# Performance work log

Hardware: AMD Instinct MI355X
Metric: run time of the kernel (lower is better)

The kernel has to match this reference:

```python
import jax, jax.numpy as jnp
import numpy as np

B, T, H, V = 32, 16, 768, 32000
EPS = 1e-5


def _conv(x, w, stride, pad):
    return jax.lax.conv_general_dilated(
        x, w, (stride, stride), [(pad, pad), (pad, pad)],
        dimension_numbers=('NCHW', 'OIHW', 'NCHW'))


def _bn(x, g, b, m, v):
    inv = g / jnp.sqrt(v + EPS)
    return x * inv[None, :, None, None] + (b - m * inv)[None, :, None, None]


def setup_inputs() -> dict:
    key = jax.random.key(0)
    ks = iter(jax.random.split(key, 48))

    def rn(shape, s=0.02):
        return s * jax.random.normal(next(ks), shape, jnp.float32)

    def bn_params(c):
        g = 1.0 + 0.1 * jax.random.normal(next(ks), (c,), jnp.float32)
        b = 0.1 * jax.random.normal(next(ks), (c,), jnp.float32)
        m = 0.1 * jax.random.normal(next(ks), (c,), jnp.float32)
        v = jax.random.uniform(next(ks), (c,), jnp.float32, 0.5, 1.5)
        return g, b, m, v

    inp = {}
    inp['images'] = jax.random.normal(next(ks), (B, 3, 224, 224), jnp.float32)
    inp['captions'] = jax.random.randint(next(ks), (B, T), 0, V)

    inp['conv1_w'] = rn((64, 3, 7, 7))
    inp['bn1_g'], inp['bn1_b'], inp['bn1_m'], inp['bn1_v'] = bn_params(64)
    inp['conv2_w'] = rn((128, 64, 3, 3))
    inp['bn2_g'], inp['bn2_b'], inp['bn2_m'], inp['bn2_v'] = bn_params(128)
    inp['conv3_w'] = rn((256, 128, 3, 3))
    inp['bn3_g'], inp['bn3_b'], inp['bn3_m'], inp['bn3_v'] = bn_params(256)
    inp['conv4_w'] = rn((H, 256, 3, 3))
    inp['bn4_g'], inp['bn4_b'], inp['bn4_m'], inp['bn4_v'] = bn_params(H)

    emb = rn((V, H), 1.0)
    inp['emb_table'] = emb.at[0].set(0.0)  # padding_idx=0 row is zero
    inp['attn_w'] = rn((H, H))             # attn_proj (no bias)
    inp['w_ih'] = rn((4 * H, 2 * H))       # LSTM input weights (i,f,g,o)
    inp['w_hh'] = rn((4 * H, H))
    inp['b_ih'] = rn((4 * H,))
    inp['b_hh'] = rn((4 * H,))
    inp['fc_w'] = rn((V, H))
    inp['fc_b'] = rn((V,))
    return inp


def _forward(images, captions, conv1_w, bn1_g, bn1_b, bn1_m, bn1_v,
             conv2_w, bn2_g, bn2_b, bn2_m, bn2_v,
             conv3_w, bn3_g, bn3_b, bn3_m, bn3_v,
             conv4_w, bn4_g, bn4_b, bn4_m, bn4_v,
             emb_table, attn_w, w_ih, w_hh, b_ih, b_hh, fc_w, fc_b):
    # ---- ResNetEncoder ----
    x = jax.nn.relu(_bn(_conv(images, conv1_w, 2, 3), bn1_g, bn1_b, bn1_m, bn1_v))
    x = jax.lax.reduce_window(x, -jnp.inf, jax.lax.max, (1, 1, 3, 3), (1, 1, 2, 2),
                              ((0, 0), (0, 0), (1, 1), (1, 1)))
    x = jax.nn.relu(_bn(_conv(x, conv2_w, 1, 1), bn2_g, bn2_b, bn2_m, bn2_v))
    x = jax.nn.relu(_bn(_conv(x, conv3_w, 2, 1), bn3_g, bn3_b, bn3_m, bn3_v))
    x = jax.nn.relu(_bn(_conv(x, conv4_w, 1, 1), bn4_g, bn4_b, bn4_m, bn4_v))
    b, c, hh, ww = x.shape
    memory = x.reshape(b, c, hh * ww).transpose(0, 2, 1)[:, :196, :]  # [B,196,H]

    # ---- LSTMAttnDecoder ----
    emb = emb_table[captions]  # [B,T,H]
    h0 = jnp.zeros((b, H), jnp.float32)
    c0 = jnp.zeros((b, H), jnp.float32)

    def step(carry, e_t):
        h, cst = carry
        q = h @ attn_w.T                                    # [B,H]
        scores = jnp.einsum('bh,bmh->bm', q, memory)        # [B,196]
        ctx = jnp.einsum('bm,bmh->bh', jax.nn.softmax(scores, axis=-1), memory)
        xin = jnp.concatenate([e_t, ctx], axis=-1)          # [B,2H]
        gates = xin @ w_ih.T + b_ih + h @ w_hh.T + b_hh     # [B,4H]
        i, f, g, o = jnp.split(gates, 4, axis=-1)
        c_new = jax.nn.sigmoid(f) * cst + jax.nn.sigmoid(i) * jnp.tanh(g)
        h_new = jax.nn.sigmoid(o) * jnp.tanh(c_new)
        logits = h_new @ fc_w.T + fc_b                      # [B,V]
        return (h_new, c_new), logits

    (hT, cT), logits = jax.lax.scan(step, (h0, c0), emb.transpose(1, 0, 2))
    logits = logits.transpose(1, 0, 2)  # [B,T,V]
    return logits, (hT[None], cT[None])


def reference(images, captions, conv1_w, bn1_g, bn1_b, bn1_m, bn1_v,
              conv2_w, bn2_g, bn2_b, bn2_m, bn2_v,
              conv3_w, bn3_g, bn3_b, bn3_m, bn3_v,
              conv4_w, bn4_g, bn4_b, bn4_m, bn4_v,
              emb_table, attn_w, w_ih, w_hh, b_ih, b_hh, fc_w, fc_b):
    return _forward(images, captions, conv1_w, bn1_g, bn1_b, bn1_m, bn1_v,
                    conv2_w, bn2_g, bn2_b, bn2_m, bn2_v,
                    conv3_w, bn3_g, bn3_b, bn3_m, bn3_v,
                    conv4_w, bn4_g, bn4_b, bn4_m, bn4_v,
                    emb_table, attn_w, w_ih, w_hh, b_ih, b_hh, fc_w, fc_b)
```

## Files before the change

### kernel.cpp

```cpp
#include <hip/hip_runtime.h>
#include <math.h>

#define NB 32
#define NT 16
#define NH 768
#define NV 32000

typedef short bf16x8 __attribute__((ext_vector_type(8)));
typedef float floatx4 __attribute__((ext_vector_type(4)));
typedef unsigned short ushort_t;

__device__ __forceinline__ float bf2f(unsigned short h) {
    unsigned u = ((unsigned)h) << 16;
    return __builtin_bit_cast(float, u);
}
__device__ __forceinline__ unsigned short f2bf(float f) {
    unsigned u = __builtin_bit_cast(unsigned, f);
    u += 0x7fffu + ((u >> 16) & 1u);
    return (unsigned short)(u >> 16);
}
__device__ __forceinline__ float sigmoidf_(float x) { return 1.f / (1.f + expf(-x)); }

__device__ __forceinline__ bf16x8 cvt8(float4 a, float4 b) {
    bf16x8 t;
    t[0] = (short)f2bf(a.x); t[1] = (short)f2bf(a.y);
    t[2] = (short)f2bf(a.z); t[3] = (short)f2bf(a.w);
    t[4] = (short)f2bf(b.x); t[5] = (short)f2bf(b.y);
    t[6] = (short)f2bf(b.z); t[7] = (short)f2bf(b.w);
    return t;
}

__global__ __launch_bounds__(256) void bn_prep4(
    const float* __restrict__ g1, const float* __restrict__ b1, const float* __restrict__ m1, const float* __restrict__ v1,
    const float* __restrict__ g2, const float* __restrict__ b2, const float* __restrict__ m2, const float* __restrict__ v2,
    const float* __restrict__ g3, const float* __restrict__ b3, const float* __restrict__ m3, const float* __restrict__ v3,
    const float* __restrict__ g4, const float* __restrict__ b4, const float* __restrict__ m4, const float* __restrict__ v4,
    float* __restrict__ s1, float* __restrict__ o1, float* __restrict__ s2, float* __restrict__ o2,
    float* __restrict__ s3, float* __restrict__ o3, float* __restrict__ s4, float* __restrict__ o4) {
    int i = blockIdx.x * 256 + threadIdx.x;
    const float *g, *b, *m, *v;
    float *s, *o;
    int c;
    if (i < 64)        { g = g1; b = b1; m = m1; v = v1; s = s1; o = o1; c = i; }
    else if (i < 192)  { g = g2; b = b2; m = m2; v = v2; s = s2; o = o2; c = i - 64; }
    else if (i < 448)  { g = g3; b = b3; m = m3; v = v3; s = s3; o = o3; c = i - 192; }
    else if (i < 1216) { g = g4; b = b4; m = m4; v = v4; s = s4; o = o4; c = i - 448; }
    else return;
    float inv = g[c] * rsqrtf(v[c] + 1e-5f);
    s[c] = inv;
    o[c] = b[c] - m[c] * inv;
}

__global__ __launch_bounds__(256) void zfill(unsigned long long* __restrict__ p, long long n) {
    long long i = (long long)blockIdx.x * 256 + threadIdx.x;
    if (i < n) p[i] = 0ULL;
}

__global__ __launch_bounds__(256) void cvt_b16rows(const float* __restrict__ src, ushort_t* __restrict__ dst,
                                                   int cols8, int ldsrc, int total8) {
    int i = blockIdx.x * 256 + threadIdx.x;
    if (i >= total8) return;
    int r = i / cols8, g = i % cols8;
    const float4* s = (const float4*)(src + (size_t)r * ldsrc + g * 8);
    float4 a = s[0], b = s[1];
    *(bf16x8*)(dst + (size_t)i * 8) = cvt8(a, b);
}

__global__ __launch_bounds__(256) void cvt_packW_conv(const float* __restrict__ w, ushort_t* __restrict__ dst,
                                                      int CIN, int total) {
    int idx = blockIdx.x * 256 + threadIdx.x;
    if (idx >= total) return;
    int e = idx & 7, lane = (idx >> 3) & 63, j = (idx >> 9) & 3;
    int r = idx >> 11;
    int KQ = CIN >> 5;
    int kq = r % KQ; r /= KQ;
    int tap = r % 9; int nt = r / 9;
    int co = nt * 64 + j * 16 + (lane & 15);
    int ci = kq * 32 + (lane >> 4) * 8 + e;
    dst[idx] = f2bf(w[((size_t)co * CIN + ci) * 9 + tap]);
}

__global__ __launch_bounds__(256) void cvt_wcombP(const float* __restrict__ w_ih, const float* __restrict__ w_hh,
                                                  ushort_t* __restrict__ dst) {
    int idx = blockIdx.x * 256 + threadIdx.x;
    if (idx >= 3072 * 1536) return;
    int e = idx & 7, lane = (idx >> 3) & 63;
    int t = idx >> 9;
    int kq = t % 48, gg = t / 48;
    int g = gg & 3, bx = gg >> 2;
    int j = g * 768 + bx * 16 + (lane & 15);
    int k = kq * 32 + (lane >> 4) * 8 + e;
    float v = (k < NH) ? w_ih[(size_t)j * (2 * NH) + NH + k] : w_hh[(size_t)j * NH + (k - NH)];
    dst[idx] = f2bf(v);
}

__global__ __launch_bounds__(256) void cvt_wattnTP(const float* __restrict__ w, ushort_t* __restrict__ dst) {
    int idx = blockIdx.x * 256 + threadIdx.x;
    if (idx >= 768 * 768) return;
    int e = idx & 7, lane = (idx >> 3) & 63, j = (idx >> 9) & 3;
    int t = idx >> 11;
    int kq = t % 24, nt = t / 24;
    int n = nt * 64 + 16 * j + (lane & 15);
    int k = kq * 32 + (lane >> 4) * 8 + e;
    dst[idx] = f2bf(w[(size_t)k * 768 + n]);
}

__global__ __launch_bounds__(256) void cvt_pad(const float* __restrict__ src, ushort_t* __restrict__ dst) {
    int idx = blockIdx.x * 256 + threadIdx.x;
    if (idx >= 64 * 160) return;
    int co = idx / 160, k = idx % 160;
    dst[idx] = (k < 147) ? f2bf(src[co * 147 + k]) : (ushort_t)0;
}

__global__ __launch_bounds__(256) void im2col1(const float* __restrict__ img, ushort_t* __restrict__ A) {
    int idx = blockIdx.x * 256 + threadIdx.x;
    const int total = 121856 * 160;
    if (idx >= total) return;
    int k = idx % 160;
    int m = idx / 160;
    ushort_t v = 0;
    if (k < 147) {
        int b = m / 3808;
        int rm = m % 3808;
        int y = rm / 112, x = rm % 112;
        int ci = k / 49;
        int r = k % 49;
        int ky = r / 7, kx = r % 7;
        int iy = 2 * y - 3 + ky;
        int ix = 2 * x - 3 + kx;
        if ((unsigned)iy < 224u && (unsigned)ix < 224u)
            v = f2bf(img[((size_t)(b * 3 + ci) * 224 + iy) * 224 + ix]);
    }
    A[idx] = v;
}

__global__ __launch_bounds__(256) void conv1_gemm(
    const ushort_t* __restrict__ A, const ushort_t* __restrict__ Bw,
    const float* __restrict__ scale, const float* __restrict__ bias,
    ushort_t* __restrict__ out) {
    int lane = threadIdx.x & 63, w = threadIdx.x >> 6;
    int m0 = (blockIdx.x * 4 + w) * 64;
    int lr = lane & 15, kl = (lane >> 4) * 8;
    floatx4 acc[4][4];
    #pragma unroll
    for (int i = 0; i < 4; ++i)
        #pragma unroll
        for (int j = 0; j < 4; ++j) acc[i][j] = 0.f;
    #pragma unroll
    for (int k0 = 0; k0 < 160; k0 += 32) {
        bf16x8 a[4], bb[4];
        #pragma unroll
        for (int i = 0; i < 4; ++i) a[i] = *(const bf16x8*)(A + (size_t)(m0 + 16 * i + lr) * 160 + kl + k0);
        #pragma unroll
        for (int j = 0; j < 4; ++j) bb[j] = *(const bf16x8*)(Bw + (size_t)(16 * j + lr) * 160 + kl + k0);
        #pragma unroll
        for (int i = 0; i < 4; ++i)
            #pragma unroll
            for (int j = 0; j < 4; ++j)
                acc[i][j] = __builtin_amdgcn_mfma_f32_16x16x32_bf16(a[i], bb[j], acc[i][j], 0, 0, 0);
    }
    #pragma unroll
    for (int i = 0; i < 4; ++i) {
        #pragma unroll
        for (int r = 0; r < 4; ++r) {
            int m = m0 + 16 * i + (lane >> 4) * 4 + r;
            int b = m / 3808;
            int rm = m % 3808;
            int y = rm / 112, x = rm % 112;
            #pragma unroll
            for (int j = 0; j < 4; ++j) {
                int n = 16 * j + lr;
                float v = fmaxf(acc[i][j][r] * scale[n] + bias[n], 0.f);
                out[((size_t)(b * 34 + y) * 112 + x) * 64 + n] = f2bf(v);
            }
        }
    }
}

__global__ __launch_bounds__(256) void pool_kernel(const ushort_t* __restrict__ in,
                                                   ushort_t* __restrict__ hal2) {
    int idx = blockIdx.x * 256 + threadIdx.x;
    const int total = 32 * 17 * 56 * 8;
    if (idx >= total) return;
    int c8 = idx & 7;
    int rest = idx >> 3;
    int x = rest % 56; rest /= 56;
    int y = rest % 17; int b = rest / 17;
    float mx[8];
    #pragma unroll
    for (int j = 0; j < 8; ++j) mx[j] = -INFINITY;
    for (int dy = -1; dy <= 1; ++dy) {
        int iy = 2 * y + dy;
        if ((unsigned)iy >= 34u) continue;
        for (int dx = -1; dx <= 1; ++dx) {
            int ix = 2 * x + dx;
            if ((unsigned)ix >= 112u) continue;
            bf16x8 v = *(const bf16x8*)(in + (((size_t)(b * 34 + iy)) * 112 + ix) * 64 + c8 * 8);
            #pragma unroll
            for (int j = 0; j < 8; ++j) mx[j] = fmaxf(mx[j], bf2f((unsigned short)v[j]));
        }
    }
    bf16x8 o;
    #pragma unroll
    for (int j = 0; j < 8; ++j) o[j] = (short)f2bf(mx[j]);
    *(bf16x8*)(hal2 + (((size_t)(b * 19 + y + 1)) * 58 + (x + 1)) * 64 + c8 * 8) = o;
}

template <int CIN, int HH, int WH, int STRIDE, int HOUT, int WOUT, int COUT, int MEMOUT, int OH, int OW>
__global__ __launch_bounds__(64) void conv_mfma(
    const ushort_t* __restrict__ in, const ushort_t* __restrict__ wtP,
    const float* __restrict__ scale, const float* __restrict__ bias,
    ushort_t* __restrict__ out) {
    int lane = threadIdx.x;
    int mt = blockIdx.x, nt = blockIdx.y;
    int lr = lane & 15, kl = (lane >> 4) * 8;
    int rowoff[4];
    #pragma unroll
    for (int i = 0; i < 4; ++i) {
        int m = mt * 64 + 16 * i + lr;
        int b = m / (HOUT * WOUT);
        int rm = m % (HOUT * WOUT);
        int y = rm / WOUT, x = rm % WOUT;
        rowoff[i] = ((b * HH + y * STRIDE) * WH + x * STRIDE) * CIN + kl;
    }
    floatx4 acc[4][4];
    #pragma unroll
    for (int i = 0; i < 4; ++i)
        #pragma unroll
        for (int j = 0; j < 4; ++j) acc[i][j] = 0.f;

    #pragma unroll
    for (int ky = 0; ky < 3; ++ky) {
        #pragma unroll
        for (int kx = 0; kx < 3; ++kx) {
            int ioff = (ky * WH + kx) * CIN;
            int t = ky * 3 + kx;
            #pragma unroll
            for (int k0 = 0; k0 < CIN; k0 += 32) {
                bf16x8 a[4], bb[4];
                #pragma unroll
                for (int i = 0; i < 4; ++i)
                    a[i] = *(const bf16x8*)(in + rowoff[i] + ioff + k0);
                #pragma unroll
                for (int j = 0; j < 4; ++j)
                    bb[j] = *(const bf16x8*)(wtP + ((((size_t)(nt * 9 + t) * (CIN / 32) + (k0 >> 5)) * 4 + j) * 64 + lane) * 8);
                #pragma unroll
                for (int i = 0; i < 4; ++i)
                    #pragma unroll
                    for (int j = 0; j < 4; ++j)
                        acc[i][j] = __builtin_amdgcn_mfma_f32_16x16x32_bf16(a[i], bb[j], acc[i][j], 0, 0, 0);
            }
        }
    }
    #pragma unroll
    for (int i = 0; i < 4; ++i) {
        #pragma unroll
        for (int r = 0; r < 4; ++r) {
            int m = mt * 64 + 16 * i + (lane >> 4) * 4 + r;
            int b = m / (HOUT * WOUT);
            int rm = m % (HOUT * WOUT);
            int y = rm / WOUT, x = rm % WOUT;
            #pragma unroll
            for (int j = 0; j < 4; ++j) {
                int n = nt * 64 + 16 * j + lr;
                float v = fmaxf(acc[i][j][r] * scale[n] + bias[n], 0.f);
                ushort_t hv = f2bf(v);
                if (MEMOUT) {
                    out[(size_t)m * COUT + n] = hv;
                } else {
                    out[((size_t)(b * OH + y + 1) * OW + (x + 1)) * COUT + n] = hv;
                }
            }
        }
    }
}

__global__ __launch_bounds__(64) void kmat_gemm(
    const ushort_t* __restrict__ memv, const ushort_t* __restrict__ Bp,
    ushort_t* __restrict__ KT) {
    int lane = threadIdx.x;
    int mt = blockIdx.x, nt = blockIdx.y;
    int lr = lane & 15, kl = (lane >> 4) * 8;
    floatx4 acc[4][4];
    #pragma unroll
    for (int i = 0; i < 4; ++i)
        #pragma unroll
        for (int j = 0; j < 4; ++j) acc[i][j] = 0.f;
    for (int kq = 0; kq < 24; ++kq) {
        bf16x8 a[4], bb[4];
        #pragma unroll
        for (int i = 0; i < 4; ++i)
            a[i] = *(const bf16x8*)(memv + (size_t)(mt * 64 + 16 * i + lr) * 768 + kq * 32 + kl);
        #pragma unroll
        for (int j = 0; j < 4; ++j)
            bb[j] = *(const bf16x8*)(Bp + (((size_t)(nt * 24 + kq) * 4 + j) * 64 + lane) * 8);
        #pragma unroll
        for (int i = 0; i < 4; ++i)
            #pragma unroll
            for (int j = 0; j < 4; ++j)
                acc[i][j] = __builtin_amdgcn_mfma_f32_16x16x32_bf16(a[i], bb[j], acc[i][j], 0, 0, 0);
    }
    #pragma unroll
    for (int i = 0; i < 4; ++i) {
        #pragma unroll
        for (int r = 0; r < 4; ++r) {
            int mg = mt * 64 + 16 * i + (lane >> 4) * 4 + r;
            int b = mg / 196, m = mg % 196;
            #pragma unroll
            for (int j = 0; j < 4; ++j) {
                int n = nt * 64 + 16 * j + lr;
                KT[(((size_t)b * 96 + (n >> 3)) * 196 + m) * 8 + (n & 7)] = f2bf(acc[i][j][r]);
            }
        }
    }
}

__global__ __launch_bounds__(256) void gather_embP(const int* __restrict__ caps,
                                                   const float* __restrict__ table,
                                                   ushort_t* __restrict__ dst) {
    int idx = blockIdx.x * 256 + threadIdx.x;
    if (idx >= 512 * 768) return;
    int e = idx & 7, lane = (idx >> 3) & 63, i = (idx >> 9) & 3;
    int t2 = idx >> 11;
    int kq = t2 % 24, mt = t2 / 24;
    int r = mt * 64 + i * 16 + (lane & 15);
    int k = kq * 32 + (lane >> 4) * 8 + e;
    int t = r >> 5, b = r & 31;
    dst[idx] = f2bf(table[(size_t)caps[b * NT + t] * NH + k]);
}

template <int REMAP>
__global__ __launch_bounds__(256, 4) void gemm_ldsb(
    const ushort_t* __restrict__ Ap, const ushort_t* __restrict__ Bb,
    const float* __restrict__ bias1, const float* __restrict__ bias2,
    float* __restrict__ C, int N) {
    __shared__ ushort_t bt[2][64 * 72];
    int tid = threadIdx.x;
    int lane = tid & 63, w = tid >> 6;
    int nt = blockIdx.x, mh = blockIdx.y;
    int n0 = nt * 64;
    int mt = mh * 4 + w;
    int lr = lane & 15, hi = lane >> 4;
    int srow = tid >> 2, sc = tid & 3;
    const ushort_t* gsrc = Bb + (size_t)(n0 + srow) * 768 + sc * 8;
    int woff = srow * 72 + sc * 8;
    floatx4 acc[4][4];
    #pragma unroll
    for (int i = 0; i < 4; ++i)
        #pragma unroll
        for (int j = 0; j < 4; ++j) acc[i][j] = 0.f;
    bf16x8 s0 = *(const bf16x8*)(gsrc);
    bf16x8 s1 = *(const bf16x8*)(gsrc + 32);
    for (int kc = 0; kc < 12; ++kc) {
        ushort_t* bufw = &bt[kc & 1][0];
        *(bf16x8*)(bufw + woff) = s0;
        *(bf16x8*)(bufw + woff + 32) = s1;
        if (kc < 11) {
            const ushort_t* p = gsrc + (size_t)(kc + 1) * 64;
            s0 = *(const bf16x8*)(p);
            s1 = *(const bf16x8*)(p + 32);
        }
        __syncthreads();
        const ushort_t* bufr = &bt[kc & 1][0];
        #pragma unroll
        for (int kk = 0; kk < 2; ++kk) {
            int kq = kc * 2 + kk;
            bf16x8 bfr[4], a[4];
            #pragma unroll
            for (int j = 0; j < 4; ++j)
                bfr[j] = *(const bf16x8*)(bufr + (j * 16 + lr) * 72 + kk * 32 + hi * 8);
            #pragma unroll
            for (int i = 0; i < 4; ++i)
                a[i] = *(const bf16x8*)(Ap + ((((size_t)mt * 24 + kq) * 4 + i) * 64 + lane) * 8);
            #pragma unroll
            for (int i = 0; i < 4; ++i)
                #pragma unroll
                for (int j = 0; j < 4; ++j)
                    acc[i][j] = __builtin_amdgcn_mfma_f32_16x16x32_bf16(a[i], bfr[j], acc[i][j], 0, 0, 0);
        }
    }
    #pragma unroll
    for (int i = 0; i < 4; ++i) {
        #pragma unroll
        for (int rr = 0; rr < 4; ++rr) {
            int m = mt * 64 + 16 * i + hi * 4 + rr;
            #pragma unroll
            for (int j = 0; j < 4; ++j) {
                int n = n0 + 16 * j + lr;
                float vv = acc[i][j][rr];
                if (bias1) vv += bias1[n];
                if (bias2) vv += bias2[n];
                if (REMAP) {
                    int t = m >> 5, b = m & 31;
                    C[(size_t)((b << 4) + t) * NV + n] = vv;
                } else {
                    C[(size_t)m * N + n] = vv;
                }
            }
        }
    }
}

__global__ __launch_bounds__(768) void attn2(
    ushort_t* __restrict__ xin, const ushort_t* __restrict__ KT,
    const ushort_t* __restrict__ mem) {
    __shared__ float hq[NH];
    __shared__ float sl[196];
    __shared__ float red[16];
    int b = blockIdx.x, tid = threadIdx.x;
    hq[tid] = bf2f(xin[(size_t)b * 1536 + NH + tid]);
    __syncthreads();
    if (tid < 392) {
        int m = tid >> 1, half = tid & 1;
        const ushort_t* basep = KT + (((size_t)b * 96 + half * 48) * 196 + m) * 8;
        float acc = 0.f;
        #pragma unroll 4
        for (int k8 = 0; k8 < 48; ++k8) {
            bf16x8 v = *(const bf16x8*)(basep + (size_t)k8 * 196 * 8);
            const float* qp = hq + (half * 48 + k8) * 8;
            #pragma unroll
            for (int j = 0; j < 8; ++j)
                acc = fmaf(bf2f((unsigned short)v[j]), qp[j], acc);
        }
        acc += __shfl_xor(acc, 1);
        if (!half) sl[m] = acc;
    }
    __syncthreads();
    float sc = (tid < 196) ? sl[tid] : -INFINITY;
    float v = sc;
    #pragma unroll
    for (int off = 32; off; off >>= 1) v = fmaxf(v, __shfl_down(v, off));
    if ((tid & 63) == 0) red[tid >> 6] = v;
    __syncthreads();
    if (tid == 0) {
        float m = red[0];
        for (int i = 1; i < 12; ++i) m = fmaxf(m, red[i]);
        red[12] = m;
    }
    __syncthreads();
    float mx = red[12];
    float e = (tid < 196) ? expf(sc - mx) : 0.f;
    __syncthreads();
    v = e;
    #pragma unroll
    for (int off = 32; off; off >>= 1) v += __shfl_down(v, off);
    if ((tid & 63) == 0) red[tid >> 6] = v;
    __syncthreads();
    if (tid == 0) {
        float s = red[0];
        for (int i = 1; i < 12; ++i) s += red[i];
        red[12] = 1.f / s;
    }
    __syncthreads();
    if (tid < 196) sl[tid] = e * red[12];
    __syncthreads();
    {
        float acc = 0.f;
        const ushort_t* mb = mem + (size_t)b * 196 * NH + tid;
        #pragma unroll 4
        for (int m = 0; m < 196; ++m) acc = fmaf(sl[m], bf2f(mb[(size_t)m * NH]), acc);
        xin[(size_t)b * 1536 + tid] = f2bf(acc);
    }
}

__global__ __launch_bounds__(256) void step_fused(
    const ushort_t* __restrict__ xin_r, const ushort_t* __restrict__ wcombP,
    const float* __restrict__ eg_t,
    float* __restrict__ cbuf, float* __restrict__ hbuf,
    ushort_t* __restrict__ xin_w, ushort_t* __restrict__ hallP, int tstep) {
    __shared__ float pbuf[4][64][33];
    int lane = threadIdx.x & 63, w = threadIdx.x >> 6;
    int bx = blockIdx.x;
    int lr = lane & 15, kl = (lane >> 4) * 8;
    floatx4 acc[2][4];
    #pragma unroll
    for (int i = 0; i < 2; ++i)
        #pragma unroll
        for (int g = 0; g < 4; ++g) acc[i][g] = 0.f;
    for (int kq = 0; kq < 12; ++kq) {
        int k = w * 384 + kq * 32;
        bf16x8 a[2], bb[4];
        #pragma unroll
        for (int i = 0; i < 2; ++i)
            a[i] = *(const bf16x8*)(xin_r + (size_t)(16 * i + lr) * 1536 + k + kl);
        #pragma unroll
        for (int g = 0; g < 4; ++g)
            bb[g] = *(const bf16x8*)(wcombP + (((size_t)(bx * 4 + g) * 48 + (w * 12 + kq)) * 64 + lane) * 8);
        #pragma unroll
        for (int i = 0; i < 2; ++i)
            #pragma unroll
            for (int g = 0; g < 4; ++g)
                acc[i][g] = __builtin_amdgcn_mfma_f32_16x16x32_bf16(a[i], bb[g], acc[i][g], 0, 0, 0);
    }
    #pragma unroll
    for (int i = 0; i < 2; ++i)
        #pragma unroll
        for (int g = 0; g < 4; ++g)
            #pragma unroll
            for (int r = 0; r < 4; ++r) {
                int m = 16 * i + (lane >> 4) * 4 + r;
                pbuf[w][g * 16 + lr][m] = acc[i][g][r];
            }
    __syncthreads();
    int tid = threadIdx.x;
    #pragma unroll
    for (int o = 0; o < 2; ++o) {
        int pid = tid * 2 + o;
        int m = pid & 31, c = pid >> 5;
        int kcol = bx * 16 + c;
        float gi = 0.f, gf = 0.f, gg = 0.f, go = 0.f;
        #pragma unroll
        for (int ww = 0; ww < 4; ++ww) {
            gi += pbuf[ww][c][m];
            gf += pbuf[ww][16 + c][m];
            gg += pbuf[ww][32 + c][m];
            go += pbuf[ww][48 + c][m];
        }
        const float* eg = eg_t + (size_t)m * 3072;
        gi += eg[kcol];
        gf += eg[768 + kcol];
        gg += eg[1536 + kcol];
        go += eg[2304 + kcol];
        float cst = cbuf[m * 768 + kcol];
        float cn = sigmoidf_(gf) * cst + sigmoidf_(gi) * tanhf(gg);
        float hn = sigmoidf_(go) * tanhf(cn);
        cbuf[m * 768 + kcol] = cn;
        hbuf[m * 768 + kcol] = hn;
        ushort_t hb = f2bf(hn);
        xin_w[(size_t)m * 1536 + NH + kcol] = hb;
        int rrow = tstep * 32 + m;
        int mtp = rrow >> 6, ip = (rrow >> 4) & 3, lrp = rrow & 15;
        int kqp = kcol >> 5, hip = (kcol >> 3) & 3, ep = kcol & 7;
        hallP[((((size_t)mtp * 24 + kqp) * 4 + ip) * 64 + (lrp | (hip << 4))) * 8 + ep] = hb;
    }
}

__global__ __launch_bounds__(256) void zero_state(float* __restrict__ h, float* __restrict__ c,
                                                  ushort_t* __restrict__ xin) {
    int i = blockIdx.x * 256 + threadIdx.x;
    if (i < NB * 1536) xin[i] = 0;
    if (i < NB * NH) { h[i] = 0.f; c[i] = 0.f; }
}

__global__ __launch_bounds__(256) void copy_hc(const float* __restrict__ h, const float* __restrict__ c,
                                               float* __restrict__ out) {
    int i = blockIdx.x * 256 + threadIdx.x;
    if (i < NB * NH) {
        out[(size_t)NB * NT * NV + i] = h[i];
        out[(size_t)NB * NT * NV + NB * NH + i] = c[i];
    }
}

extern "C" void kernel_launch(void* const* d_in, const int* in_sizes, int n_in,
                              void* d_out, int out_size, void* d_ws, size_t ws_size,
                              hipStream_t stream) {
    const float* images   = (const float*)d_in[0];
    const int*   captions = (const int*)d_in[1];
    const float* conv1_w  = (const float*)d_in[2];
    const float* bn1_g = (const float*)d_in[3], *bn1_b = (const float*)d_in[4];
    const float* bn1_m = (const float*)d_in[5], *bn1_v = (const float*)d_in[6];
    const float* conv2_w  = (const float*)d_in[7];
    const float* bn2_g = (const float*)d_in[8], *bn2_b = (const float*)d_in[9];
    const float* bn2_m = (const float*)d_in[10], *bn2_v = (const float*)d_in[11];
    const float* conv3_w  = (const float*)d_in[12];
    const float* bn3_g = (const float*)d_in[13], *bn3_b = (const float*)d_in[14];
    const float* bn3_m = (const float*)d_in[15], *bn3_v = (const float*)d_in[16];
    const float* conv4_w  = (const float*)d_in[17];
    const float* bn4_g = (const float*)d_in[18], *bn4_b = (const float*)d_in[19];
    const float* bn4_m = (const float*)d_in[20], *bn4_v = (const float*)d_in[21];
    const float* emb_table = (const float*)d_in[22];
    const float* attn_w   = (const float*)d_in[23];
    const float* w_ih     = (const float*)d_in[24];
    const float* w_hh     = (const float*)d_in[25];
    const float* b_ih     = (const float*)d_in[26];
    const float* b_hh     = (const float*)d_in[27];
    const float* fc_w     = (const float*)d_in[28];
    const float* fc_b     = (const float*)d_in[29];
    float* out = (float*)d_out;

    char* base = (char*)d_ws;
    size_t off = 0;
    auto alloc = [&](size_t bytes) { char* p = base + off; off += (bytes + 255) & ~(size_t)255; return p; };
    float* s1 = (float*)alloc(64 * 4);   float* bb1 = (float*)alloc(64 * 4);
    float* s2 = (float*)alloc(128 * 4);  float* bb2 = (float*)alloc(128 * 4);
    float* s3 = (float*)alloc(256 * 4);  float* bb3 = (float*)alloc(256 * 4);
    float* s4 = (float*)alloc(768 * 4);  float* bb4 = (float*)alloc(768 * 4);
    ushort_t* c1out = (ushort_t*)alloc((size_t)32 * 34 * 112 * 64 * 2);
    size_t halo_start = off;
    ushort_t* hal2 = (ushort_t*)alloc((size_t)32 * 19 * 58 * 64 * 2);
    ushort_t* hal3 = (ushort_t*)alloc((size_t)32 * 18 * 58 * 128 * 2);
    ushort_t* hal4 = (ushort_t*)alloc((size_t)32 * 10 * 30 * 256 * 2);
    size_t halo_bytes = off - halo_start;
    ushort_t* memv = (ushort_t*)alloc((size_t)32 * 196 * 768 * 2);
    ushort_t* KT   = (ushort_t*)alloc((size_t)32 * 96 * 196 * 8 * 2);
    ushort_t* wb1 = (ushort_t*)alloc((size_t)64 * 160 * 2);
    ushort_t* wb2 = (ushort_t*)alloc((size_t)128 * 9 * 64 * 2);
    ushort_t* wb3 = (ushort_t*)alloc((size_t)256 * 9 * 128 * 2);
    ushort_t* wb4 = (ushort_t*)alloc((size_t)768 * 9 * 256 * 2);
    ushort_t* wattnTP = (ushort_t*)alloc((size_t)768 * 768 * 2);
    ushort_t* wcombP = (ushort_t*)alloc((size_t)3072 * 1536 * 2);
    ushort_t* wihL = (ushort_t*)alloc((size_t)3072 * 768 * 2);
    ushort_t* e512P = (ushort_t*)alloc((size_t)512 * 768 * 2);
    float* eg   = (float*)alloc((size_t)512 * 3072 * 4);
    ushort_t* HallP = (ushort_t*)alloc((size_t)512 * 768 * 2);
    float* hbuf = (float*)alloc(NB * NH * 4);
    float* cbuf = (float*)alloc(NB * NH * 4);
    ushort_t* xinA = (ushort_t*)alloc((size_t)NB * 1536 * 2);
    ushort_t* xinB = (ushort_t*)alloc((size_t)NB * 1536 * 2);
    char* ubig = alloc((size_t)NV * NH * 2);
    ushort_t* imcol = (ushort_t*)ubig;
    ushort_t* fcwb  = (ushort_t*)ubig;

    bn_prep4<<<5, 256, 0, stream>>>(bn1_g, bn1_b, bn1_m, bn1_v,
                                    bn2_g, bn2_b, bn2_m, bn2_v,
                                    bn3_g, bn3_b, bn3_m, bn3_v,
                                    bn4_g, bn4_b, bn4_m, bn4_v,
                                    s1, bb1, s2, bb2, s3, bb3, s4, bb4);
    cvt_pad<<<(64 * 160 + 255) / 256, 256, 0, stream>>>(conv1_w, wb1);
    cvt_packW_conv<<<(128 * 9 * 64 + 255) / 256, 256, 0, stream>>>(conv2_w, wb2, 64, 128 * 9 * 64);
    cvt_packW_conv<<<(256 * 9 * 128 + 255) / 256, 256, 0, stream>>>(conv3_w, wb3, 128, 256 * 9 * 128);
    cvt_packW_conv<<<(768 * 9 * 256 + 255) / 256, 256, 0, stream>>>(conv4_w, wb4, 256, 768 * 9 * 256);
    cvt_wattnTP<<<(768 * 768 + 255) / 256, 256, 0, stream>>>(attn_w, wattnTP);
    cvt_wcombP<<<(3072 * 1536 + 255) / 256, 256, 0, stream>>>(w_ih, w_hh, wcombP);
    cvt_b16rows<<<(3072 * 96 + 255) / 256, 256, 0, stream>>>(w_ih, wihL, 96, 1536, 3072 * 96);
    {
        long long n8 = (long long)(halo_bytes / 8);
        zfill<<<(unsigned)((n8 + 255) / 256), 256, 0, stream>>>((unsigned long long*)hal2, n8);
    }

    im2col1<<<(121856 * 160 + 255) / 256, 256, 0, stream>>>(images, imcol);
    conv1_gemm<<<476, 256, 0, stream>>>(imcol, wb1, s1, bb1, c1out);
    cvt_b16rows<<<(NV * 96 + 255) / 256, 256, 0, stream>>>(fc_w, fcwb, 96, 768, NV * 96);
    pool_kernel<<<(32 * 17 * 56 * 8 + 255) / 256, 256, 0, stream>>>(c1out, hal2);
    conv_mfma<64, 19, 58, 1, 16, 56, 128, 0, 18, 58>
        <<<dim3(448, 2), 64, 0, stream>>>(hal2, wb2, s2, bb2, hal3);
    conv_mfma<128, 18, 58, 2, 8, 28, 256, 0, 10, 30>
        <<<dim3(112, 4), 64, 0, stream>>>(hal3, wb3, s3, bb3, hal4);
    conv_mfma<256, 10, 30, 1, 7, 28, 768, 1, 1, 1>
        <<<dim3(98, 12), 64, 0, stream>>>(hal4, wb4, s4, bb4, memv);

    kmat_gemm<<<dim3(98, 12), 64, 0, stream>>>(memv, wattnTP, KT);

    gather_embP<<<(512 * 768) / 256, 256, 0, stream>>>(captions, emb_table, e512P);
    gemm_ldsb<0><<<dim3(48, 2), 256, 0, stream>>>(e512P, wihL, b_ih, b_hh, eg, 3072);
    zero_state<<<(NB * 1536 + 255) / 256, 256, 0, stream>>>(hbuf, cbuf, xinA);

    ushort_t* xcur = xinA;
    ushort_t* xnxt = xinB;
    for (int t = 0; t < NT; ++t) {
        attn2<<<NB, NH, 0, stream>>>(xcur, KT, memv);
        step_fused<<<48, 256, 0, stream>>>(
            xcur, wcombP, eg + (size_t)t * NB * 3072, cbuf, hbuf, xnxt, HallP, t);
        ushort_t* tmp = xcur; xcur = xnxt; xnxt = tmp;
    }

    gemm_ldsb<1><<<dim3(500, 2), 256, 0, stream>>>(HallP, fcwb, fc_b, nullptr, out, NV);

    copy_hc<<<(NB * NH + 255) / 256, 256, 0, stream>>>(hbuf, cbuf, out);
}
```

Baseline: 904.4 us.

## Fuse decoder timestep loop into one cooperative persistent kernel; pack conv waves per block

```diff
diff --git a/kernel.cpp b/kernel.cpp
--- a/kernel.cpp
+++ b/kernel.cpp
@@ -1,5 +1,8 @@
 #include <hip/hip_runtime.h>
+#include <hip/hip_cooperative_groups.h>
 #include <math.h>
+
+namespace cg = cooperative_groups;
 
 #define NB 32
 #define NT 16
@@ -169,7 +172,8 @@
             int y = rm / 112, x = rm % 112;
             #pragma unroll
             for (int j = 0; j < 4; ++j) {
-                int n = 16 * j + lr;
+                int n = 16 * j + lane & 15 ? 16 * j + (lane & 15) : 16 * j + (lane & 15);
+                n = 16 * j + (lane & 15);
                 float v = fmaxf(acc[i][j][r] * scale[n] + bias[n], 0.f);
                 out[((size_t)(b * 34 + y) * 112 + x) * 64 + n] = f2bf(v);
             }
@@ -207,12 +211,15 @@
 }
 
 template <int CIN, int HH, int WH, int STRIDE, int HOUT, int WOUT, int COUT, int MEMOUT, int OH, int OW>
-__global__ __launch_bounds__(64) void conv_mfma(
+__global__ __launch_bounds__(256) void conv_mfma(
     const ushort_t* __restrict__ in, const ushort_t* __restrict__ wtP,
     const float* __restrict__ scale, const float* __restrict__ bias,
     ushort_t* __restrict__ out) {
-    int lane = threadIdx.x;
-    int mt = blockIdx.x, nt = blockIdx.y;
+    const int MT = (32 * HOUT * WOUT) / 64;
+    int lane = threadIdx.x & 63, w = threadIdx.x >> 6;
+    int mt = blockIdx.x * 4 + w;
+    if (mt >= MT) return;
+    int nt = blockIdx.y;
     int lr = lane & 15, kl = (lane >> 4) * 8;
     int rowoff[4];
     #pragma unroll
@@ -275,11 +282,13 @@
     }
 }
 
-__global__ __launch_bounds__(64) void kmat_gemm(
+__global__ __launch_bounds__(256) void kmat_gemm(
     const ushort_t* __restrict__ memv, const ushort_t* __restrict__ Bp,
     ushort_t* __restrict__ KT) {
-    int lane = threadIdx.x;
-    int mt = blockIdx.x, nt = blockIdx.y;
+    int lane = threadIdx.x & 63, w = threadIdx.x >> 6;
+    int mt = blockIdx.x * 4 + w;
+    if (mt >= 98) return;
+    int nt = blockIdx.y;
     int lr = lane & 15, kl = (lane >> 4) * 8;
     floatx4 acc[4][4];
     #pragma unroll
@@ -401,137 +410,138 @@
     }
 }
 
-__global__ __launch_bounds__(768) void attn2(
-    ushort_t* __restrict__ xin, const ushort_t* __restrict__ KT,
-    const ushort_t* __restrict__ mem) {
+__global__ __launch_bounds__(256) void decoder_persist(
+    ushort_t* __restrict__ xinA, ushort_t* __restrict__ xinB,
+    const ushort_t* __restrict__ wcombP, const ushort_t* __restrict__ KT,
+    const ushort_t* __restrict__ mem, const float* __restrict__ eg,
+    float* __restrict__ cbuf, float* __restrict__ hbuf,
+    ushort_t* __restrict__ hallP) {
+    cg::grid_group grid = cg::this_grid();
+    __shared__ float pbuf[4][64][33];
     __shared__ float hq[NH];
     __shared__ float sl[196];
     __shared__ float red[16];
-    int b = blockIdx.x, tid = threadIdx.x;
-    hq[tid] = bf2f(xin[(size_t)b * 1536 + NH + tid]);
-    __syncthreads();
-    if (tid < 392) {
-        int m = tid >> 1, half = tid & 1;
-        const ushort_t* basep = KT + (((size_t)b * 96 + half * 48) * 196 + m) * 8;
-        float acc = 0.f;
-        #pragma unroll 4
-        for (int k8 = 0; k8 < 48; ++k8) {
-            bf16x8 v = *(const bf16x8*)(basep + (size_t)k8 * 196 * 8);
-            const float* qp = hq + (half * 48 + k8) * 8;
-            #pragma unroll
-            for (int j = 0; j < 8; ++j)
-                acc = fmaf(bf2f((unsigned short)v[j]), qp[j], acc);
-        }
-        acc += __shfl_xor(acc, 1);
-        if (!half) sl[m] = acc;
-    }
-    __syncthreads();
-    float sc = (tid < 196) ? sl[tid] : -INFINITY;
-    float v = sc;
-    #pragma unroll
-    for (int off = 32; off; off >>= 1) v = fmaxf(v, __shfl_down(v, off));
-    if ((tid & 63) == 0) red[tid >> 6] = v;
-    __syncthreads();
-    if (tid == 0) {
-        float m = red[0];
-        for (int i = 1; i < 12; ++i) m = fmaxf(m, red[i]);
-        red[12] = m;
-    }
-    __syncthreads();
-    float mx = red[12];
-    float e = (tid < 196) ? expf(sc - mx) : 0.f;
-    __syncthreads();
-    v = e;
-    #pragma unroll
-    for (int off = 32; off; off >>= 1) v += __shfl_down(v, off);
-    if ((tid & 63) == 0) red[tid >> 6] = v;
-    __syncthreads();
-    if (tid == 0) {
-        float s = red[0];
-        for (int i = 1; i < 12; ++i) s += red[i];
-        red[12] = 1.f / s;
-    }
-    __syncthreads();
-    if (tid < 196) sl[tid] = e * red[12];
-    __syncthreads();
-    {
-        float acc = 0.f;
-        const ushort_t* mb = mem + (size_t)b * 196 * NH + tid;
-        #pragma unroll 4
-        for (int m = 0; m < 196; ++m) acc = fmaf(sl[m], bf2f(mb[(size_t)m * NH]), acc);
-        xin[(size_t)b * 1536 + tid] = f2bf(acc);
-    }
-}
-
-__global__ __launch_bounds__(256) void step_fused(
-    const ushort_t* __restrict__ xin_r, const ushort_t* __restrict__ wcombP,
-    const float* __restrict__ eg_t,
-    float* __restrict__ cbuf, float* __restrict__ hbuf,
-    ushort_t* __restrict__ xin_w, ushort_t* __restrict__ hallP, int tstep) {
-    __shared__ float pbuf[4][64][33];
-    int lane = threadIdx.x & 63, w = threadIdx.x >> 6;
     int bx = blockIdx.x;
+    int tid = threadIdx.x;
+    int lane = tid & 63, w = tid >> 6;
     int lr = lane & 15, kl = (lane >> 4) * 8;
-    floatx4 acc[2][4];
-    #pragma unroll
-    for (int i = 0; i < 2; ++i)
-        #pragma unroll
-        for (int g = 0; g < 4; ++g) acc[i][g] = 0.f;
-    for (int kq = 0; kq < 12; ++kq) {
-        int k = w * 384 + kq * 32;
-        bf16x8 a[2], bb[4];
-        #pragma unroll
-        for (int i = 0; i < 2; ++i)
-            a[i] = *(const bf16x8*)(xin_r + (size_t)(16 * i + lr) * 1536 + k + kl);
-        #pragma unroll
-        for (int g = 0; g < 4; ++g)
-            bb[g] = *(const bf16x8*)(wcombP + (((size_t)(bx * 4 + g) * 48 + (w * 12 + kq)) * 64 + lane) * 8);
-        #pragma unroll
-        for (int i = 0; i < 2; ++i)
-            #pragma unroll
-            for (int g = 0; g < 4; ++g)
-                acc[i][g] = __builtin_amdgcn_mfma_f32_16x16x32_bf16(a[i], bb[g], acc[i][g], 0, 0, 0);
-    }
-    #pragma unroll
-    for (int i = 0; i < 2; ++i)
-        #pragma unroll
-        for (int g = 0; g < 4; ++g)
-            #pragma unroll
-            for (int r = 0; r < 4; ++r) {
-                int m = 16 * i + (lane >> 4) * 4 + r;
-                pbuf[w][g * 16 + lr][m] = acc[i][g][r];
-            }
-    __syncthreads();
-    int tid = threadIdx.x;
-    #pragma unroll
-    for (int o = 0; o < 2; ++o) {
-        int pid = tid * 2 + o;
-        int m = pid & 31, c = pid >> 5;
-        int kcol = bx * 16 + c;
-        float gi = 0.f, gf = 0.f, gg = 0.f, go = 0.f;
-        #pragma unroll
-        for (int ww = 0; ww < 4; ++ww) {
-            gi += pbuf[ww][c][m];
-            gf += pbuf[ww][16 + c][m];
-            gg += pbuf[ww][32 + c][m];
-            go += pbuf[ww][48 + c][m];
-        }
-        const float* eg = eg_t + (size_t)m * 3072;
-        gi += eg[kcol];
-        gf += eg[768 + kcol];
-        gg += eg[1536 + kcol];
-        go += eg[2304 + kcol];
-        float cst = cbuf[m * 768 + kcol];
-        float cn = sigmoidf_(gf) * cst + sigmoidf_(gi) * tanhf(gg);
-        float hn = sigmoidf_(go) * tanhf(cn);
-        cbuf[m * 768 + kcol] = cn;
-        hbuf[m * 768 + kcol] = hn;
-        ushort_t hb = f2bf(hn);
-        xin_w[(size_t)m * 1536 + NH + kcol] = hb;
-        int rrow = tstep * 32 + m;
-        int mtp = rrow >> 6, ip = (rrow >> 4) & 3, lrp = rrow & 15;
-        int kqp = kcol >> 5, hip = (kcol >> 3) & 3, ep = kcol & 7;
-        hallP[((((size_t)mtp * 24 + kqp) * 4 + ip) * 64 + (lrp | (hip << 4))) * 8 + ep] = hb;
+    ushort_t* xcur = xinA;
+    ushort_t* xnxt = xinB;
+    for (int t = 0; t < NT; ++t) {
+        if (bx < 32) {
+            int b = bx;
+            for (int i = tid; i < NH; i += 256) hq[i] = bf2f(xcur[(size_t)b * 1536 + NH + i]);
+            __syncthreads();
+            if (tid < 196) {
+                const ushort_t* basep = KT + ((size_t)b * 96 * 196 + tid) * 8;
+                float acc = 0.f;
+                #pragma unroll 4
+                for (int k8 = 0; k8 < 96; ++k8) {
+                    bf16x8 v = *(const bf16x8*)(basep + (size_t)k8 * 196 * 8);
+                    const float* qp = hq + k8 * 8;
+                    #pragma unroll
+                    for (int j = 0; j < 8; ++j)
+                        acc = fmaf(bf2f((unsigned short)v[j]), qp[j], acc);
+                }
+                sl[tid] = acc;
+            }
+            __syncthreads();
+            float sc = (tid < 196) ? sl[tid] : -INFINITY;
+            float v = sc;
+            #pragma unroll
+            for (int off = 32; off; off >>= 1) v = fmaxf(v, __shfl_down(v, off));
+            if ((tid & 63) == 0) red[tid >> 6] = v;
+            __syncthreads();
+            if (tid == 0) {
+                float mm = fmaxf(fmaxf(red[0], red[1]), fmaxf(red[2], red[3]));
+                red[8] = mm;
+            }
+            __syncthreads();
+            float mx = red[8];
+            float e = (tid < 196) ? expf(sc - mx) : 0.f;
+            v = e;
+            #pragma unroll
+            for (int off = 32; off; off >>= 1) v += __shfl_down(v, off);
+            if ((tid & 63) == 0) red[tid >> 6] = v;
+            __syncthreads();
+            if (tid == 0) red[8] = 1.f / (red[0] + red[1] + red[2] + red[3]);
+            __syncthreads();
+            if (tid < 196) sl[tid] = e * red[8];
+            __syncthreads();
+            for (int j = tid; j < NH; j += 256) {
+                float acc = 0.f;
+                const ushort_t* mb = mem + (size_t)b * 196 * NH + j;
+                #pragma unroll 4
+                for (int m = 0; m < 196; ++m) acc = fmaf(sl[m], bf2f(mb[(size_t)m * NH]), acc);
+                xcur[(size_t)b * 1536 + j] = f2bf(acc);
+            }
+        }
+        grid.sync();
+        {
+            const float* eg_t = eg + (size_t)t * NB * 3072;
+            floatx4 acc[2][4];
+            #pragma unroll
+            for (int i = 0; i < 2; ++i)
+                #pragma unroll
+                for (int g = 0; g < 4; ++g) acc[i][g] = 0.f;
+            for (int kq = 0; kq < 12; ++kq) {
+                int k = w * 384 + kq * 32;
+                bf16x8 a[2], bb[4];
+                #pragma unroll
+                for (int i = 0; i < 2; ++i)
+                    a[i] = *(const bf16x8*)(xcur + (size_t)(16 * i + lr) * 1536 + k + kl);
+                #pragma unroll
+                for (int g = 0; g < 4; ++g)
+                    bb[g] = *(const bf16x8*)(wcombP + (((size_t)(bx * 4 + g) * 48 + (w * 12 + kq)) * 64 + lane) * 8);
+                #pragma unroll
+                for (int i = 0; i < 2; ++i)
+                    #pragma unroll
+                    for (int g = 0; g < 4; ++g)
+                        acc[i][g] = __builtin_amdgcn_mfma_f32_16x16x32_bf16(a[i], bb[g], acc[i][g], 0, 0, 0);
+            }
+            #pragma unroll
+            for (int i = 0; i < 2; ++i)
+                #pragma unroll
+                for (int g = 0; g < 4; ++g)
+                    #pragma unroll
+                    for (int r = 0; r < 4; ++r) {
+                        int m = 16 * i + (lane >> 4) * 4 + r;
+                        pbuf[w][g * 16 + lr][m] = acc[i][g][r];
+                    }
+            __syncthreads();
+            #pragma unroll
+            for (int o = 0; o < 2; ++o) {
+                int pid = tid * 2 + o;
+                int m = pid & 31, c = pid >> 5;
+                int kcol = bx * 16 + c;
+                float gi = 0.f, gf = 0.f, gg = 0.f, go = 0.f;
+                #pragma unroll
+                for (int ww = 0; ww < 4; ++ww) {
+                    gi += pbuf[ww][c][m];
+                    gf += pbuf[ww][16 + c][m];
+                    gg += pbuf[ww][32 + c][m];
+                    go += pbuf[ww][48 + c][m];
+                }
+                const float* egp = eg_t + (size_t)m * 3072;
+                gi += egp[kcol];
+                gf += egp[768 + kcol];
+                gg += egp[1536 + kcol];
+                go += egp[2304 + kcol];
+                float cst = cbuf[m * 768 + kcol];
+                float cn = sigmoidf_(gf) * cst + sigmoidf_(gi) * tanhf(gg);
+                float hn = sigmoidf_(go) * tanhf(cn);
+                cbuf[m * 768 + kcol] = cn;
+                hbuf[m * 768 + kcol] = hn;
+                ushort_t hb = f2bf(hn);
+                xnxt[(size_t)m * 1536 + NH + kcol] = hb;
+                int rrow = t * 32 + m;
+                int mtp = rrow >> 6, ip = (rrow >> 4) & 3, lrp = rrow & 15;
+                int kqp = kcol >> 5, hip = (kcol >> 3) & 3, ep = kcol & 7;
+                hallP[((((size_t)mtp * 24 + kqp) * 4 + ip) * 64 + (lrp | (hip << 4))) * 8 + ep] = hb;
+            }
+        }
+        grid.sync();
+        ushort_t* tmp = xcur; xcur = xnxt; xnxt = tmp;
     }
 }
 
@@ -633,25 +643,22 @@
     cvt_b16rows<<<(NV * 96 + 255) / 256, 256, 0, stream>>>(fc_w, fcwb, 96, 768, NV * 96);
     pool_kernel<<<(32 * 17 * 56 * 8 + 255) / 256, 256, 0, stream>>>(c1out, hal2);
     conv_mfma<64, 19, 58, 1, 16, 56, 128, 0, 18, 58>
-        <<<dim3(448, 2), 64, 0, stream>>>(hal2, wb2, s2, bb2, hal3);
+        <<<dim3(112, 2), 256, 0, stream>>>(hal2, wb2, s2, bb2, hal3);
     conv_mfma<128, 18, 58, 2, 8, 28, 256, 0, 10, 30>
-        <<<dim3(112, 4), 64, 0, stream>>>(hal3, wb3, s3, bb3, hal4);
+        <<<dim3(28, 4), 256, 0, stream>>>(hal3, wb3, s3, bb3, hal4);
     conv_mfma<256, 10, 30, 1, 7, 28, 768, 1, 1, 1>
-        <<<dim3(98, 12), 64, 0, stream>>>(hal4, wb4, s4, bb4, memv);
-
-    kmat_gemm<<<dim3(98, 12), 64, 0, stream>>>(memv, wattnTP, KT);
+        <<<dim3(25, 12), 256, 0, stream>>>(hal4, wb4, s4, bb4, memv);
+
+    kmat_gemm<<<dim3(25, 12), 256, 0, stream>>>(memv, wattnTP, KT);
 
     gather_embP<<<(512 * 768) / 256, 256, 0, stream>>>(captions, emb_table, e512P);
     gemm_ldsb<0><<<dim3(48, 2), 256, 0, stream>>>(e512P, wihL, b_ih, b_hh, eg, 3072);
     zero_state<<<(NB * 1536 + 255) / 256, 256, 0, stream>>>(hbuf, cbuf, xinA);
 
-    ushort_t* xcur = xinA;
-    ushort_t* xnxt = xinB;
-    for (int t = 0; t < NT; ++t) {
-        attn2<<<NB, NH, 0, stream>>>(xcur, KT, memv);
-        step_fused<<<48, 256, 0, stream>>>(
-            xcur, wcombP, eg + (size_t)t * NB * 3072, cbuf, hbuf, xnxt, HallP, t);
-        ushort_t* tmp = xcur; xcur = xnxt; xnxt = tmp;
+    {
+        void* args[] = {&xinA, &xinB, &wcombP, &KT, &memv, &eg, &cbuf, &hbuf, &HallP};
+        hipLaunchCooperativeKernel((const void*)decoder_persist, dim3(48), dim3(256),
+                                   args, 0, stream);
     }
 
     gemm_ldsb<1><<<dim3(500, 2), 256, 0, stream>>>(HallP, fcwb, fc_b, nullptr, out, NV);
```

Result: slower. 1.819 ms (+101.2%).
